# Performance work log

Hardware: AMD Instinct MI355X
Metric: run time of the kernel (lower is better)

## Reference

```python
import math
import jax, jax.numpy as jnp
import numpy as np

N_FEATURES = 32
DEGREE = 3
BATCH = 8192
N_POLY = math.comb(N_FEATURES + DEGREE, DEGREE)  # 6545


def _build_monomial_indices(n_features, degree):
    """Static (numpy) indices replicating the Pascal-triangle recursion in TaylorMap._poly.

    For degree level i (i = 1..degree-1), the original code appends, for each feature f,
    x[:, f] * prev_block[:, :comb(i+f, i)].  We flatten that into gather index arrays so the
    whole block is one vectorized gather+multiply instead of a Python loop of slices/concats.
    """
    levels = []
    for i in range(1, degree):
        counts = np.array([math.comb(i + f, i) for f in range(n_features)], dtype=np.int64)
        f_idx = np.repeat(np.arange(n_features, dtype=np.int64), counts)
        m_idx = np.concatenate([np.arange(c, dtype=np.int64) for c in counts])
        levels.append((f_idx, m_idx))
    return levels

_LEVELS = _build_monomial_indices(N_FEATURES, DEGREE)


def _poly(x):
    # x: [B, n].  Returns [B, n_poly] monomial features in the exact order of TaylorMap._poly.
    b = x.shape[0]
    parts = [jnp.ones((b, 1), x.dtype), x]
    prev = x
    for f_idx, m_idx in _LEVELS:  # static loop over degree levels (degree-1 iterations)
        new = x[:, f_idx] * prev[:, m_idx]  # [B, comb(n+i, i+1)-ish block]
        parts.append(new)
        prev = new
    return jnp.concatenate(parts, axis=-1)


def setup_inputs() -> dict:
    key = jax.random.key(0)
    kx, kw = jax.random.split(key)
    x = jax.random.normal(kx, (BATCH, N_FEATURES), dtype=jnp.float32)
    # learned weight W: [n_poly, n_features] (default init is zeros; use small randn for a
    # non-degenerate numerical baseline)
    W = jax.random.normal(kw, (N_POLY, N_FEATURES), dtype=jnp.float32) * 0.02
    return {"x": x, "W": W}


def reference(x, W):
    # TaylorMap(x) = x * residual + poly(x) @ W   (residual=True)
    return x + _poly(x) @ W
```

## Files before the change

kernel.cpp:

```cpp
#include <hip/hip_runtime.h>
#include <cstdint>
#include <cstddef>
#include <utility>


#define NF 32
#define NPOLY 6545
#define NSTEPS 448
#define NREAL 417
#define NOCT 834
#define NDESC 1024
#define CHUNK 28
#define TSTRIDE 576
#define D2OFF 40
#define XDSTRIDE 34

#define XD_OFF    36864
#define SMEM_BYTES 39040

typedef _Float16 f16x8 __attribute__((ext_vector_type(8)));
typedef float f32x16 __attribute__((ext_vector_type(16)));

#define D2N 528
struct D2I { uint8_t a[D2N]; uint8_t b[D2N]; };
constexpr D2I build_d2i() {
    D2I t{};
    int k = 0;
    for (int f = 0; f < NF; ++f)
        for (int m = 0; m <= f; ++m) { t.a[k] = (uint8_t)f; t.b[k] = (uint8_t)m; ++k; }
    return t;
}
constexpr D2I D2T = build_d2i();

struct Desc { uint32_t d[NDESC]; };
constexpr Desc build_desc() {
    Desc D{};
    int u = 0;
    for (int o = 0; o < 72; ++o)
        D.d[u++] = (uint32_t)(o * 16);
    for (int f = 0; f < NF; ++f) {
        int cnt = (f + 1) * (f + 2) / 2;
        for (int j8 = 0; j8 < (cnt + 7) / 8; ++j8)
            D.d[u++] = (uint32_t)((D2OFF + 8 * j8) * 2) | ((uint32_t)((1 + f) * 2) << 16);
    }
    while (u < NDESC) D.d[u++] = 0u;
    return D;
}
__device__ const Desc DESC_G = build_desc();

struct Oldk { int16_t v[NSTEPS * 16]; };
constexpr Oldk build_oldk() {
    Oldk K{};
    int k = 0;
    for (int ti = 0; ti < 576; ++ti) {
        int old;
        if (ti == 0) old = 0;
        else if (ti <= 32) old = ti;
        else if (ti >= D2OFF && ti < D2OFF + D2N) old = 33 + (ti - D2OFF);
        else old = -1;
        K.v[k++] = (int16_t)old;
    }
    for (int f = 0; f < NF; ++f) {
        int cnt = (f + 1) * (f + 2) / 2;
        int off3 = 0;
        for (int g = 0; g < f; ++g) off3 += (g + 1) * (g + 2) / 2;
        int oc = (cnt + 7) / 8;
        for (int m = 0; m < oc * 8; ++m)
            K.v[k++] = (int16_t)(m < cnt ? 561 + off3 + m : -1);
    }
    while (k < NSTEPS * 16) K.v[k++] = (int16_t)-1;
    return K;
}
__device__ const Oldk OLDK_G = build_oldk();

template<int TI>
__device__ __forceinline__ _Float16 tval(const float (&xr)[NF]) {
    if constexpr (TI == 0) return (_Float16)1.0f;
    else if constexpr (TI >= 1 && TI <= 32) return (_Float16)xr[TI - 1];
    else if constexpr (TI >= D2OFF && TI < D2OFF + D2N) {
        constexpr int m = TI - D2OFF;
        return (_Float16)(xr[D2T.a[m]] * xr[D2T.b[m]]);
    } else return (_Float16)0.0f;
}

template<int O, int... Js>
__device__ __forceinline__ void put_oct(std::integer_sequence<int, Js...>,
                                        const float (&xr)[NF], _Float16* trow, int r) {
    f16x8 v = { tval<O * 8 + Js>(xr)... };
    int slot = (O & ~7) | ((O ^ r) & 7);
    *(f16x8*)(trow + slot * 8) = v;
}

template<int BASE, int... Os>
__device__ __forceinline__ void p1_octs(std::integer_sequence<int, Os...>,
                                        const float (&xr)[NF], _Float16* trow, int r) {
    (put_oct<BASE + Os>(std::make_integer_sequence<int, 8>{}, xr, trow, r), ...);
}

template<int V>
__device__ __forceinline__ void xdw(const float (&xr)[NF], _Float16* xdrow) {
    if constexpr (V == 0) xdrow[0] = (_Float16)1.0f;
    else if constexpr (V <= 32) xdrow[V] = (_Float16)xr[V - 1];
}

template<int G>
__device__ __forceinline__ void p1_group(const float (&xr)[NF], _Float16* trow,
                                         _Float16* xdrow, int r) {
    if constexpr (G < 8)
        p1_octs<G * 5>(std::make_integer_sequence<int, 5>{}, xr, trow, r);
    else
        p1_octs<40 + (G - 8) * 4>(std::make_integer_sequence<int, 4>{}, xr, trow, r);
    xdw<2 * G>(xr, xdrow);
    xdw<2 * G + 1>(xr, xdrow);
    if constexpr (G == 15) xdw<32>(xr, xdrow);
}

__global__ void prep(const float* __restrict__ x, const float* __restrict__ W,
                     float* __restrict__ out, _Float16* __restrict__ Wh) {
    int b = blockIdx.x;
    if (b < 256) {
        int id = b * 256 + threadIdx.x;
        ((float4*)out)[id] = ((const float4*)x)[id];
    } else {
        int id = (b - 256) * 256 + threadIdx.x;
        if (id < NSTEPS * 64) {
            int step = id >> 6, rem = id & 63, hs = rem >> 5, n = rem & 31;
            int k0 = step * 16 + hs * 8;
            f16x8 v;
#pragma unroll
            for (int j = 0; j < 8; ++j) {
                int old = OLDK_G.v[k0 + j];
                v[j] = (_Float16)(old >= 0 ? W[old * 32 + n] : 0.0f);
            }
            *(f16x8*)(Wh + (size_t)id * 8) = v;
        }
    }
}

__global__ __launch_bounds__(512, 4) void gemm(const float* __restrict__ x,
                                               const _Float16* __restrict__ Wh,
                                               float* __restrict__ out) {
    __shared__ __align__(16) unsigned char smem[SMEM_BYTES];
    _Float16* t  = (_Float16*)smem;
    _Float16* xd = (_Float16*)(smem + XD_OFF);

    const int tid = threadIdx.x;
    const int wave = __builtin_amdgcn_readfirstlane(tid >> 6);
    const int lane = tid & 63;
    const int hsel = lane >> 5, r = lane & 31;
    const int mtile = blockIdx.x >> 1;
    const int kh = blockIdx.x & 1;

    {
        const int pr = tid & 31, g = tid >> 5;
        float xr[NF];
        const float4* xp = (const float4*)(x + (size_t)(mtile * 32 + pr) * NF);
#pragma unroll
        for (int i = 0; i < 8; ++i) {
            float4 v = xp[i];
            xr[4 * i + 0] = v.x; xr[4 * i + 1] = v.y;
            xr[4 * i + 2] = v.z; xr[4 * i + 3] = v.w;
        }
        _Float16* trow = t + pr * TSTRIDE;
        _Float16* xdrow = xd + pr * XDSTRIDE;
        switch (g) {
            case  0: p1_group< 0>(xr, trow, xdrow, pr); break;
            case  1: p1_group< 1>(xr, trow, xdrow, pr); break;
            case  2: p1_group< 2>(xr, trow, xdrow, pr); break;
            case  3: p1_group< 3>(xr, trow, xdrow, pr); break;
            case  4: p1_group< 4>(xr, trow, xdrow, pr); break;
            case  5: p1_group< 5>(xr, trow, xdrow, pr); break;
            case  6: p1_group< 6>(xr, trow, xdrow, pr); break;
            case  7: p1_group< 7>(xr, trow, xdrow, pr); break;
            case  8: p1_group< 8>(xr, trow, xdrow, pr); break;
            case  9: p1_group< 9>(xr, trow, xdrow, pr); break;
            case 10: p1_group<10>(xr, trow, xdrow, pr); break;
            case 11: p1_group<11>(xr, trow, xdrow, pr); break;
            case 12: p1_group<12>(xr, trow, xdrow, pr); break;
            case 13: p1_group<13>(xr, trow, xdrow, pr); break;
            case 14: p1_group<14>(xr, trow, xdrow, pr); break;
            default: p1_group<15>(xr, trow, xdrow, pr); break;
        }
    }

    const int c = kh * 8 + wave;
    const int s0 = __builtin_amdgcn_readfirstlane(c * CHUNK);
    uint32_t vD0 = DESC_G.d[2 * (s0 + lane)];
    uint32_t vD1 = DESC_G.d[2 * (s0 + lane) + 1];

    __syncthreads();

    const char* trowB = (const char*)t + r * (TSTRIDE * 2);
    const char* xdrowB = (const char*)xd + r * (XDSTRIDE * 2);
    const char* wpB = (const char*)Wh + lane * 16;
    const uint32_t rx = (uint32_t)((r & 7) << 4);

    f32x16 acc;
#pragma unroll
    for (int i = 0; i < 16; ++i) acc[i] = 0.0f;

#define DSEL(IDX) (hsel ? __builtin_amdgcn_readlane(vD1, (IDX)) \
                        : __builtin_amdgcn_readlane(vD0, (IDX)))

    f16x8 araw0, araw1, araw2, araw3;
    f16x8 breg0, breg1, breg2, breg3;
    _Float16 xs0, xs1, xs2, xs3;

#define LOADSLOT(P, IDX) do {                                                 \
    uint32_t d_ = DSEL(IDX);                                                  \
    araw##P = *(const f16x8*)(trowB + ((d_ & 0xffffu) ^ rx));                 \
    xs##P   = *(const _Float16*)(xdrowB + (d_ >> 16));                        \
    breg##P = *(const f16x8*)(wpB + (size_t)(s0 + (IDX)) * 1024);             \
} while (0)

    LOADSLOT(0, 0); LOADSLOT(1, 1); LOADSLOT(2, 2); LOADSLOT(3, 3);

#define BODY(P, IDX) do {                                                     \
    f16x8 xsv_ = { xs##P, xs##P, xs##P, xs##P, xs##P, xs##P, xs##P, xs##P };  \
    f16x8 a_ = araw##P * xsv_;                                                \
    f16x8 bu_ = breg##P;                                                      \
    LOADSLOT(P, (IDX) + 4);   \
    acc = __builtin_amdgcn_mfma_f32_32x32x16_f16(a_, bu_, acc, 0, 0, 0);      \
} while (0)

#pragma unroll
    for (int i = 0; i < 7; ++i) {
        BODY(0, 4 * i + 0);
        BODY(1, 4 * i + 1);
        BODY(2, 4 * i + 2);
        BODY(3, 4 * i + 3);
    }
#undef BODY
#undef LOADSLOT
#undef DSEL

    __syncthreads();
    float* red = (float*)smem;
    float* bank = red + wave * 1024;
#pragma unroll
    for (int reg = 0; reg < 16; ++reg) {
        int rr = (reg & 3) + 8 * (reg >> 2) + 4 * hsel;
        bank[rr * 32 + r] = acc[reg];
    }
    __syncthreads();
    float* op = out + (size_t)mtile * 1024;
#pragma unroll
    for (int i = 0; i < 2; ++i) {
        int e = tid + i * 512;
        float v = red[e] + red[1024 + e] + red[2048 + e] + red[3072 + e]
                + red[4096 + e] + red[5120 + e] + red[6144 + e] + red[7168 + e];
        atomicAdd(op + e, v);
    }
}

extern "C" void kernel_launch(void* const* d_in, const int* in_sizes, int n_in,
                              void* d_out, int out_size, void* d_ws, size_t ws_size,
                              hipStream_t stream) {
    (void)in_sizes; (void)n_in; (void)out_size; (void)ws_size;
    const float* x = (const float*)d_in[0];
    const float* W = (const float*)d_in[1];
    float* out = (float*)d_out;
    _Float16* Wh = (_Float16*)d_ws;

    prep<<<368, 256, 0, stream>>>(x, W, out, Wh);
    gemm<<<512, 512, 0, stream>>>(x, Wh, out);
}
```

Before: 70.11 us.

## Drop K-split across blocks, write output directly, add dual accumulators

Each GEMM block now covers the full K range (CHUNK doubled, 256 blocks instead of 512), so the atomicAdd split-K reduction and the out=x copy in prep are removed and the residual x is added in the epilogue with a plain store. The MFMA loop uses two accumulators and an 8-deep load pipeline to break the accumulator dependency chain, and prep now only converts W, reading its gather indices as vector loads. The trade-off is half as many blocks, each doing twice the work, with lower occupancy (launch bounds 2) and more registers per thread.

```diff
diff --git a/kernel.cpp b/kernel.cpp
--- a/kernel.cpp
+++ b/kernel.cpp
@@ -10,7 +10,7 @@
 #define NREAL 417
 #define NOCT 834
 #define NDESC 1024
-#define CHUNK 28
+#define CHUNK 56
 #define TSTRIDE 576
 #define D2OFF 40
 #define XDSTRIDE 34
@@ -20,6 +20,7 @@
 
 typedef _Float16 f16x8 __attribute__((ext_vector_type(8)));
 typedef float f32x16 __attribute__((ext_vector_type(16)));
+typedef short short8v __attribute__((ext_vector_type(8)));
 
 #define D2N 528
 struct D2I { uint8_t a[D2N]; uint8_t b[D2N]; };
@@ -115,29 +116,21 @@
     if constexpr (G == 15) xdw<32>(xr, xdrow);
 }
 
-__global__ void prep(const float* __restrict__ x, const float* __restrict__ W,
-                     float* __restrict__ out, _Float16* __restrict__ Wh) {
-    int b = blockIdx.x;
-    if (b < 256) {
-        int id = b * 256 + threadIdx.x;
-        ((float4*)out)[id] = ((const float4*)x)[id];
-    } else {
-        int id = (b - 256) * 256 + threadIdx.x;
-        if (id < NSTEPS * 64) {
-            int step = id >> 6, rem = id & 63, hs = rem >> 5, n = rem & 31;
-            int k0 = step * 16 + hs * 8;
-            f16x8 v;
-#pragma unroll
-            for (int j = 0; j < 8; ++j) {
-                int old = OLDK_G.v[k0 + j];
-                v[j] = (_Float16)(old >= 0 ? W[old * 32 + n] : 0.0f);
-            }
-            *(f16x8*)(Wh + (size_t)id * 8) = v;
-        }
-    }
-}
-
-__global__ __launch_bounds__(512, 4) void gemm(const float* __restrict__ x,
+__global__ void prep(const float* __restrict__ W, _Float16* __restrict__ Wh) {
+    int id = blockIdx.x * 256 + threadIdx.x;
+    int step = id >> 6, rem = id & 63, hs = rem >> 5, n = rem & 31;
+    int k0 = step * 16 + hs * 8;
+    short8v olds = *(const short8v*)(OLDK_G.v + k0);
+    f16x8 v;
+#pragma unroll
+    for (int j = 0; j < 8; ++j) {
+        int old = olds[j];
+        v[j] = (_Float16)(old >= 0 ? W[old * 32 + n] : 0.0f);
+    }
+    *(f16x8*)(Wh + (size_t)id * 8) = v;
+}
+
+__global__ __launch_bounds__(512, 2) void gemm(const float* __restrict__ x,
                                                const _Float16* __restrict__ Wh,
                                                float* __restrict__ out) {
     __shared__ __align__(16) unsigned char smem[SMEM_BYTES];
@@ -148,8 +141,7 @@
     const int wave = __builtin_amdgcn_readfirstlane(tid >> 6);
     const int lane = tid & 63;
     const int hsel = lane >> 5, r = lane & 31;
-    const int mtile = blockIdx.x >> 1;
-    const int kh = blockIdx.x & 1;
+    const int mtile = blockIdx.x;
 
     {
         const int pr = tid & 31, g = tid >> 5;
@@ -183,8 +175,7 @@
         }
     }
 
-    const int c = kh * 8 + wave;
-    const int s0 = __builtin_amdgcn_readfirstlane(c * CHUNK);
+    const int s0 = __builtin_amdgcn_readfirstlane(wave * CHUNK);
     uint32_t vD0 = DESC_G.d[2 * (s0 + lane)];
     uint32_t vD1 = DESC_G.d[2 * (s0 + lane) + 1];
 
@@ -195,16 +186,16 @@
     const char* wpB = (const char*)Wh + lane * 16;
     const uint32_t rx = (uint32_t)((r & 7) << 4);
 
-    f32x16 acc;
-#pragma unroll
-    for (int i = 0; i < 16; ++i) acc[i] = 0.0f;
+    f32x16 acc0, acc1;
+#pragma unroll
+    for (int i = 0; i < 16; ++i) { acc0[i] = 0.0f; acc1[i] = 0.0f; }
 
 #define DSEL(IDX) (hsel ? __builtin_amdgcn_readlane(vD1, (IDX)) \
                         : __builtin_amdgcn_readlane(vD0, (IDX)))
 
-    f16x8 araw0, araw1, araw2, araw3;
-    f16x8 breg0, breg1, breg2, breg3;
-    _Float16 xs0, xs1, xs2, xs3;
+    f16x8 araw0, araw1, araw2, araw3, araw4, araw5, araw6, araw7;
+    f16x8 breg0, breg1, breg2, breg3, breg4, breg5, breg6, breg7;
+    _Float16 xs0, xs1, xs2, xs3, xs4, xs5, xs6, xs7;
 
 #define LOADSLOT(P, IDX) do {                                                 \
     uint32_t d_ = DSEL(IDX);                                                  \
@@ -214,42 +205,52 @@
 } while (0)
 
     LOADSLOT(0, 0); LOADSLOT(1, 1); LOADSLOT(2, 2); LOADSLOT(3, 3);
-
-#define BODY(P, IDX) do {                                                     \
+    LOADSLOT(4, 4); LOADSLOT(5, 5); LOADSLOT(6, 6); LOADSLOT(7, 7);
+
+#define BODY(P, IDX, A) do {                                                  \
     f16x8 xsv_ = { xs##P, xs##P, xs##P, xs##P, xs##P, xs##P, xs##P, xs##P };  \
     f16x8 a_ = araw##P * xsv_;                                                \
     f16x8 bu_ = breg##P;                                                      \
-    LOADSLOT(P, (IDX) + 4);   \
-    acc = __builtin_amdgcn_mfma_f32_32x32x16_f16(a_, bu_, acc, 0, 0, 0);      \
+    LOADSLOT(P, (IDX) + 8);   \
+    A = __builtin_amdgcn_mfma_f32_32x32x16_f16(a_, bu_, A, 0, 0, 0);          \
 } while (0)
 
 #pragma unroll
     for (int i = 0; i < 7; ++i) {
-        BODY(0, 4 * i + 0);
-        BODY(1, 4 * i + 1);
-        BODY(2, 4 * i + 2);
-        BODY(3, 4 * i + 3);
+        BODY(0, 8 * i + 0, acc0);
+        BODY(1, 8 * i + 1, acc1);
+        BODY(2, 8 * i + 2, acc0);
+        BODY(3, 8 * i + 3, acc1);
+        BODY(4, 8 * i + 4, acc0);
+        BODY(5, 8 * i + 5, acc1);
+        BODY(6, 8 * i + 6, acc0);
+        BODY(7, 8 * i + 7, acc1);
     }
 #undef BODY
 #undef LOADSLOT
 #undef DSEL
 
+#pragma unroll
+    for (int i = 0; i < 16; ++i) acc0[i] += acc1[i];
+
     __syncthreads();
     float* red = (float*)smem;
     float* bank = red + wave * 1024;
 #pragma unroll
     for (int reg = 0; reg < 16; ++reg) {
         int rr = (reg & 3) + 8 * (reg >> 2) + 4 * hsel;
-        bank[rr * 32 + r] = acc[reg];
+        bank[rr * 32 + r] = acc0[reg];
     }
     __syncthreads();
+    const float* xt = x + (size_t)mtile * 1024;
     float* op = out + (size_t)mtile * 1024;
 #pragma unroll
     for (int i = 0; i < 2; ++i) {
         int e = tid + i * 512;
         float v = red[e] + red[1024 + e] + red[2048 + e] + red[3072 + e]
-                + red[4096 + e] + red[5120 + e] + red[6144 + e] + red[7168 + e];
-        atomicAdd(op + e, v);
+                + red[4096 + e] + red[5120 + e] + red[6144 + e] + red[7168 + e]
+                + xt[e];
+        op[e] = v;
     }
 }
 
@@ -262,6 +263,6 @@
     float* out = (float*)d_out;
     _Float16* Wh = (_Float16*)d_ws;
 
-    prep<<<368, 256, 0, stream>>>(x, W, out, Wh);
-    gemm<<<512, 512, 0, stream>>>(x, Wh, out);
-}
+    prep<<<112, 256, 0, stream>>>(W, Wh);
+    gemm<<<256, 512, 0, stream>>>(x, Wh, out);
+}
```

Result: faster. 67.67 us (median of 2 runs) (-3.5%).
